# Kernel tuning notes

Hardware: AMD Instinct MI355X
Metric: run time of the kernel (lower is better)

Reference implementation:

```python
import jax, jax.numpy as jnp
import numpy as np

GROUPS = 8
NUM_HEADS = 8
EPS = 1e-5


def setup_inputs() -> dict:
    key = jax.random.key(0)
    ks = jax.random.split(key, 3)
    C = 512
    x = jax.random.normal(ks[0], (2, C, 64, 64), dtype=jnp.float32)
    norm_w = jnp.ones((C,), jnp.float32)
    norm_b = jnp.zeros((C,), jnp.float32)
    qkv_w = jax.random.normal(ks[1], (3 * C, C), dtype=jnp.float32) * (C ** -0.5)
    qkv_b = jnp.zeros((3 * C,), jnp.float32)
    proj_w = jax.random.normal(ks[2], (C, C), dtype=jnp.float32) * (C ** -0.5)
    proj_b = jnp.zeros((C,), jnp.float32)
    return {"x": x, "norm_w": norm_w, "norm_b": norm_b,
            "qkv_w": qkv_w, "qkv_b": qkv_b,
            "proj_w": proj_w, "proj_b": proj_b}


def reference(x, norm_w, norm_b, qkv_w, qkv_b, proj_w, proj_b):
    b, c, h, w = x.shape
    n = h * w
    hd = c // NUM_HEADS

    # GroupNorm(8, c): normalize over (channels-in-group, h, w)
    xg = x.reshape(b, GROUPS, c // GROUPS, h, w)
    mean = jnp.mean(xg, axis=(2, 3, 4), keepdims=True)
    var = jnp.var(xg, axis=(2, 3, 4), keepdims=True)
    xg = (xg - mean) * jax.lax.rsqrt(var + EPS)
    x_norm = xg.reshape(b, c, h, w) * norm_w[None, :, None, None] + norm_b[None, :, None, None]

    x_flat = x_norm.reshape(b, c, n)  # (b, c, n)
    # 1x1 Conv1d == channel-wise linear
    qkv = jnp.einsum('oc,bcn->bon', qkv_w, x_flat) + qkv_b[None, :, None]
    q, k, v = jnp.split(qkv, 3, axis=1)
    q = q.reshape(b, NUM_HEADS, hd, n)
    k = k.reshape(b, NUM_HEADS, hd, n)
    v = v.reshape(b, NUM_HEADS, hd, n)

    attn = jnp.einsum('bhdn,bhdm->bhnm', q, k) * (hd ** -0.5)  # (b,h,n,n)
    attn = jax.nn.softmax(attn, axis=-1)
    out = jnp.einsum('bhnm,bhdm->bhdn', attn, v).reshape(b, c, n)

    out = jnp.einsum('oc,bcn->bon', proj_w, out) + proj_b[None, :, None]
    return x + out.reshape(b, c, h, w)
```

## Files before the change

### kernel.cpp

```cpp
#include <hip/hip_runtime.h>
#include <stdint.h>

#define B_   2
#define C_   512
#define N_   4096
#define G_   8
#define NH_  8
#define HD_  64
#define GRPELEMS ((C_ / G_) * N_)
#define NCHUNK 64

typedef __bf16 bf16x8 __attribute__((ext_vector_type(8)));
typedef float  f32x4  __attribute__((ext_vector_type(4)));

#if __has_builtin(__builtin_amdgcn_exp2f)
#define EXP2(x) __builtin_amdgcn_exp2f(x)
#else
#define EXP2(x) exp2f(x)
#endif

__device__ inline unsigned f2bf(float f) {
    union { float f; unsigned u; } v; v.f = f;
    return (v.u + 0x7FFFu + ((v.u >> 16) & 1u)) >> 16;
}
__device__ inline __bf16 tobf(float f) {
    unsigned short u = (unsigned short)f2bf(f);
    union { unsigned short u; __bf16 b; } c; c.u = u;
    return c.b;
}
__device__ inline unsigned pktrunc(float f0, float f1) {
    return __builtin_amdgcn_perm(__float_as_uint(f1), __float_as_uint(f0),
                                 0x07060302u);
}

#define GLOAD16(g, l)                                                     \
    __builtin_amdgcn_global_load_lds(                                     \
        (const __attribute__((address_space(1))) unsigned*)(g),           \
        (__attribute__((address_space(3))) unsigned*)(l), 16, 0, 0)

__global__ __launch_bounds__(256) void gn_part(const float* __restrict__ x,
                                               float* __restrict__ psum,
                                               float* __restrict__ psq) {
    const int blk = blockIdx.x;
    const float4* p = (const float4*)x + (size_t)blk * 1024;
    const int t = threadIdx.x;
    float s = 0.f, s2 = 0.f;
#pragma unroll
    for (int i = 0; i < 4; ++i) {
        float4 v = p[t + (i << 8)];
        s  += v.x + v.y + v.z + v.w;
        s2 += v.x * v.x + v.y * v.y + v.z * v.z + v.w * v.w;
    }
#pragma unroll
    for (int off = 1; off < 64; off <<= 1) {
        s  += __shfl_xor(s, off);
        s2 += __shfl_xor(s2, off);
    }
    __shared__ float rs[4], rq[4];
    if ((t & 63) == 0) { rs[t >> 6] = s; rq[t >> 6] = s2; }
    __syncthreads();
    if (t == 0) {
        psum[blk] = rs[0] + rs[1] + rs[2] + rs[3];
        psq[blk]  = rq[0] + rq[1] + rq[2] + rq[3];
    }
}

__global__ __launch_bounds__(256) void w2bf(const float* __restrict__ qw,
                                            const float* __restrict__ pw,
                                            __bf16* __restrict__ dq,
                                            __bf16* __restrict__ dp) {
    const int QW4 = (3 * C_ * C_) / 4;
    int idx = blockIdx.x * 256 + threadIdx.x;
    float4 v; __bf16* dst; int o;
    if (idx < QW4) { v = ((const float4*)qw)[idx]; dst = dq; o = idx; }
    else           { v = ((const float4*)pw)[idx - QW4]; dst = dp; o = idx - QW4; }
    uint2 pk;
    pk.x = f2bf(v.x) | (f2bf(v.y) << 16);
    pk.y = f2bf(v.z) | (f2bf(v.w) << 16);
    *(uint2*)(dst + (size_t)o * 4) = pk;
}

__global__ __launch_bounds__(256) void gn_apply_t(const float* __restrict__ x,
                                                  const float* __restrict__ w,
                                                  const float* __restrict__ bb,
                                                  const float* __restrict__ psum,
                                                  const float* __restrict__ psq,
                                                  __bf16* __restrict__ xnT) {
    const int p0 = blockIdx.x << 6, c0 = blockIdx.y << 6, b = blockIdx.z;
    __shared__ __bf16 T[64][76];
    __shared__ float red[2 * NCHUNK];
    __shared__ float smr[2];
    const int tid = threadIdx.x;
    const int bg = b * G_ + (c0 >> 6);

    if (tid < NCHUNK)            red[tid] = psum[bg * NCHUNK + tid];
    else if (tid < 2 * NCHUNK)   red[tid] = psq[bg * NCHUNK + tid - NCHUNK];
    __syncthreads();
    if (tid == 0) {
        float s = 0.f, q = 0.f;
#pragma unroll
        for (int i = 0; i < NCHUNK; ++i) { s += red[i]; q += red[NCHUNK + i]; }
        const float inv = 1.f / (float)GRPELEMS;
        float mean = s * inv;
        float var  = q * inv - mean * mean;
        smr[0] = mean;
        smr[1] = rsqrtf(var + 1e-5f);
    }
    __syncthreads();
    const float mean = smr[0], rstd = smr[1];

    const int tr  = tid >> 4;
    const int tc4 = (tid & 15) << 2;
    const float* xb = x + ((size_t)b * C_ + c0) * N_ + p0;
#pragma unroll
    for (int cc = tr; cc < 64; cc += 16) {
        int c = c0 + cc;
        float sc = rstd * w[c];
        float sh = bb[c] - mean * sc;
        float4 v = *(const float4*)(xb + (size_t)cc * N_ + tc4);
        T[tc4 + 0][cc] = tobf(v.x * sc + sh);
        T[tc4 + 1][cc] = tobf(v.y * sc + sh);
        T[tc4 + 2][cc] = tobf(v.z * sc + sh);
        T[tc4 + 3][cc] = tobf(v.w * sc + sh);
    }
    __syncthreads();
    __bf16* dst = xnT + ((size_t)b * N_ + p0) * C_ + c0;
#pragma unroll
    for (int pp = tr; pp < 64; pp += 16)
        *(uint2*)(dst + (size_t)pp * C_ + tc4) = *(const uint2*)&T[pp][tc4];
}

template <int M_TOTAL, int EPI>
__global__ __launch_bounds__(256) void gemm_bf16(const __bf16* __restrict__ A,
                                                 const __bf16* __restrict__ Bm,
                                                 const float* __restrict__ bias,
                                                 const float* __restrict__ resid,
                                                 __bf16* __restrict__ qT,
                                                 __bf16* __restrict__ kT,
                                                 __bf16* __restrict__ vB,
                                                 float* __restrict__ Y) {
    const int b  = blockIdx.z;
    const int M0 = blockIdx.y << 7;
    const int N0 = blockIdx.x << 7;
    const int tid = threadIdx.x;
    const int w = tid >> 6, lane = tid & 63;
    const int quad = lane >> 4, l16 = lane & 15;
    const int wr = w >> 1, wc = w & 1;

    __shared__ __bf16 As[128 * 64];
    __shared__ __bf16 Bs[128 * 64];

    const __bf16* Bb = Bm + (size_t)b * ((size_t)N_ * C_);

    const int srow = lane >> 3;
    const int sg   = lane & 7;

    f32x4 acc[4][4];
#pragma unroll
    for (int mt = 0; mt < 4; ++mt)
#pragma unroll
        for (int nt = 0; nt < 4; ++nt) acc[mt][nt] = (f32x4){0.f, 0.f, 0.f, 0.f};

    for (int k0 = 0; k0 < C_; k0 += 64) {
        __syncthreads();
#pragma unroll
        for (int i = 0; i < 4; ++i) {
            int r  = (w << 5) + (i << 3) + srow;
            int gc = ((sg ^ (r & 7)) << 3);
            const __bf16* ga = A  + (size_t)(M0 + r) * C_ + k0 + gc;
            const __bf16* gb = Bb + (size_t)(N0 + r) * C_ + k0 + gc;
            GLOAD16(ga, As + (((w << 2) + i) << 9));
            GLOAD16(gb, Bs + (((w << 2) + i) << 9));
        }
        __syncthreads();

#pragma unroll
        for (int kk = 0; kk < 2; ++kk) {
            bf16x8 af[4], bfr[4];
            const int gk = (kk << 2) + quad;
#pragma unroll
            for (int mt = 0; mt < 4; ++mt) {
                int m = (wr << 6) + (mt << 4) + l16;
                af[mt] = *(const bf16x8*)&As[(m << 6) + ((gk ^ (m & 7)) << 3)];
            }
#pragma unroll
            for (int nt = 0; nt < 4; ++nt) {
                int n = (wc << 6) + (nt << 4) + l16;
                bfr[nt] = *(const bf16x8*)&Bs[(n << 6) + ((gk ^ (n & 7)) << 3)];
            }
#pragma unroll
            for (int mt = 0; mt < 4; ++mt)
#pragma unroll
                for (int nt = 0; nt < 4; ++nt)
                    acc[mt][nt] = __builtin_amdgcn_mfma_f32_16x16x32_bf16(
                        af[mt], bfr[nt], acc[mt][nt], 0, 0, 0);
        }
    }

    if (EPI == 0) {
        const int t = M0 >> 9;
        const float sc = (t == 0) ? (0.125f * 1.44269504f) : 1.f;
#pragma unroll
        for (int mt = 0; mt < 4; ++mt) {
            const int o0 = M0 + (wr << 6) + (mt << 4) + (quad << 2);
            const int h  = (o0 >> 6) & 7;
            const int d0 = o0 & 63;
            const size_t bh = (size_t)b * NH_ + h;
            float bi[4];
#pragma unroll
            for (int r = 0; r < 4; ++r) bi[r] = bias[o0 + r];
            if (t < 2) {
                __bf16* dst = (t == 0 ? qT : kT) + (bh * N_) * HD_ + d0;
#pragma unroll
                for (int nt = 0; nt < 4; ++nt) {
                    int p = N0 + (wc << 6) + (nt << 4) + l16;
                    f32x4 v = acc[mt][nt];
                    uint2 pk;
                    pk.x = f2bf((v[0] + bi[0]) * sc) | (f2bf((v[1] + bi[1]) * sc) << 16);
                    pk.y = f2bf((v[2] + bi[2]) * sc) | (f2bf((v[3] + bi[3]) * sc) << 16);
                    *(uint2*)(dst + (size_t)p * HD_) = pk;
                }
            } else {
                __bf16* dst = vB + bh * ((size_t)HD_ * N_);
#pragma unroll
                for (int nt = 0; nt < 4; ++nt) {
                    int p = N0 + (wc << 6) + (nt << 4) + l16;
                    f32x4 v = acc[mt][nt];
#pragma unroll
                    for (int r = 0; r < 4; ++r)
                        dst[(size_t)(d0 + r) * N_ + p] = tobf(v[r] + bi[r]);
                }
            }
        }
    } else {
#pragma unroll
        for (int mt = 0; mt < 4; ++mt) {
            const int o0 = M0 + (wr << 6) + (mt << 4) + (quad << 2);
            float bi[4];
#pragma unroll
            for (int r = 0; r < 4; ++r) bi[r] = bias[o0 + r];
#pragma unroll
            for (int nt = 0; nt < 4; ++nt) {
                int p = N0 + (wc << 6) + (nt << 4) + l16;
                f32x4 v = acc[mt][nt];
#pragma unroll
                for (int r = 0; r < 4; ++r) {
                    size_t off = ((size_t)b * C_ + o0 + r) * N_ + p;
                    Y[off] = v[r] + bi[r] + resid[off];
                }
            }
        }
    }
}

__global__ __launch_bounds__(256) void attn_mfma(const __bf16* __restrict__ qT,
                                                 const __bf16* __restrict__ kT,
                                                 const __bf16* __restrict__ vB,
                                                 __bf16* __restrict__ attT) {
    const int tid  = threadIdx.x;
    const int w    = tid >> 6;
    const int lane = tid & 63;
    const int quad = lane >> 4;
    const int l16  = lane & 15;
    const int l7   = l16 & 7;
    const int h = blockIdx.y, b = blockIdx.z;
    const int qw0 = (blockIdx.x << 7) + (w << 5);

    __shared__ __bf16 Ks[2][64][64];
    __shared__ __bf16 Vs[2][80][64];
    __shared__ __bf16 Ps[4][32][64];

    const size_t bh = (size_t)b * NH_ + h;
    const __bf16* qTb = qT + bh * ((size_t)N_ * HD_);
    const __bf16* kTb = kT + bh * ((size_t)N_ * HD_);
    const __bf16* vBb = vB + bh * ((size_t)HD_ * N_);

    {
        int r = tid >> 3;
        int c = (tid & 7) << 3;
        __bf16 val = ((r & 15) == 0) ? (__bf16)1.0f : (__bf16)0.0f;
        __bf16* dst = &Vs[r >> 4][64 + (r & 15)][c];
#pragma unroll
        for (int u = 0; u < 8; ++u) dst[u] = val;
    }

    bf16x8 qf[2][2];
#pragma unroll
    for (int qt = 0; qt < 2; ++qt)
#pragma unroll
        for (int hh = 0; hh < 2; ++hh)
            qf[qt][hh] = *(const bf16x8*)(qTb +
                (size_t)(qw0 + (qt << 4) + l16) * HD_ + (hh << 5) + (quad << 3));

    const int rrel = lane >> 3;
    const int gsw  = ((lane & 7) ^ rrel) << 3;

    auto stage = [&](int it, int buf) {
        const int kb = it << 6;
#pragma unroll
        for (int c = 0; c < 2; ++c) {
            const int rb = (w << 4) + (c << 3);
            const __bf16* gk = kTb + (size_t)(kb + rb + rrel) * HD_ + gsw;
            GLOAD16(gk, &Ks[buf][rb][0]);
            const __bf16* gv = vBb + (size_t)(rb + rrel) * N_ + kb + gsw;
            GLOAD16(gv, &Vs[buf][rb][0]);
        }
    };

    const f32x4 zero4 = {0.f, 0.f, 0.f, 0.f};
    f32x4 o[5][2];
#pragma unroll
    for (int dt = 0; dt < 5; ++dt) { o[dt][0] = zero4; o[dt][1] = zero4; }

    stage(0, 0);

    for (int it = 0; it < 64; ++it) {
        const int cur = it & 1;
        __syncthreads();
        if (it < 63) stage(it + 1, cur ^ 1);

        f32x4 s[4][2];
#pragma unroll
        for (int kt = 0; kt < 4; ++kt) { s[kt][0] = zero4; s[kt][1] = zero4; }
#pragma unroll
        for (int hh = 0; hh < 2; ++hh) {
#pragma unroll
            for (int kt = 0; kt < 4; ++kt) {
                bf16x8 a = *(const bf16x8*)&Ks[cur][(kt << 4) + l16]
                                              [(((hh << 2) + quad) ^ l7) << 3];
                s[kt][0] = __builtin_amdgcn_mfma_f32_16x16x32_bf16(a, qf[0][hh], s[kt][0], 0, 0, 0);
                s[kt][1] = __builtin_amdgcn_mfma_f32_16x16x32_bf16(a, qf[1][hh], s[kt][1], 0, 0, 0);
            }
        }

#pragma unroll
        for (int qt = 0; qt < 2; ++qt)
#pragma unroll
            for (int kt = 0; kt < 4; ++kt) {
                f32x4 sv = s[kt][qt];
                float e0 = EXP2(sv[0]), e1 = EXP2(sv[1]);
                float e2 = EXP2(sv[2]), e3 = EXP2(sv[3]);
                uint2 pk;
                pk.x = pktrunc(e0, e1);
                pk.y = pktrunc(e2, e3);
                *(uint2*)&Ps[w][(qt << 4) + l16]
                            [(((kt << 2) + quad) ^ (l7 << 1)) << 2] = pk;
            }

#pragma unroll
        for (int hh = 0; hh < 2; ++hh) {
            bf16x8 pf0 = *(const bf16x8*)&Ps[w][l16]
                          [(((hh << 3) + (quad << 1)) ^ (l7 << 1)) << 2];
            bf16x8 pf1 = *(const bf16x8*)&Ps[w][16 + l16]
                          [(((hh << 3) + (quad << 1)) ^ (l7 << 1)) << 2];
#pragma unroll
            for (int dt = 0; dt < 5; ++dt) {
                bf16x8 a = *(const bf16x8*)&Vs[cur][(dt << 4) + l16]
                                              [(((hh << 2) + quad) ^ l7) << 3];
                o[dt][0] = __builtin_amdgcn_mfma_f32_16x16x32_bf16(a, pf0, o[dt][0], 0, 0, 0);
                o[dt][1] = __builtin_amdgcn_mfma_f32_16x16x32_bf16(a, pf1, o[dt][1], 0, 0, 0);
            }
        }
    }

    float lq[2];
    lq[0] = __shfl(o[4][0][0], l16, 64);
    lq[1] = __shfl(o[4][1][0], l16, 64);

#pragma unroll
    for (int qt = 0; qt < 2; ++qt) {
        float inv = 1.f / lq[qt];
        int n = qw0 + (qt << 4) + l16;
        __bf16* dst = attT + ((size_t)b * N_ + n) * C_ + h * HD_ + (quad << 2);
#pragma unroll
        for (int dt = 0; dt < 4; ++dt) {
            uint2 pk;
            pk.x = f2bf(o[dt][qt][0] * inv) | (f2bf(o[dt][qt][1] * inv) << 16);
            pk.y = f2bf(o[dt][qt][2] * inv) | (f2bf(o[dt][qt][3] * inv) << 16);
            *(uint2*)(dst + (dt << 4)) = pk;
        }
    }
}

extern "C" void kernel_launch(void* const* d_in, const int* in_sizes, int n_in,
                              void* d_out, int out_size, void* d_ws, size_t ws_size,
                              hipStream_t stream) {
    const float* x      = (const float*)d_in[0];
    const float* norm_w = (const float*)d_in[1];
    const float* norm_b = (const float*)d_in[2];
    const float* qkv_w  = (const float*)d_in[3];
    const float* qkv_b  = (const float*)d_in[4];
    const float* proj_w = (const float*)d_in[5];
    const float* proj_b = (const float*)d_in[6];
    float* out = (float*)d_out;

    const size_t BCN = (size_t)B_ * C_ * N_;
    float* psum  = (float*)d_ws;
    float* psq   = psum + 1024;
    __bf16* xnT  = (__bf16*)(psq + 1024);
    __bf16* qT   = xnT + BCN;
    __bf16* kT   = qT + BCN;
    __bf16* vB   = kT + BCN;
    __bf16* attT = vB + BCN;
    __bf16* wq   = attT + BCN;
    __bf16* wp   = wq + (size_t)3 * C_ * C_;

    gn_part<<<B_ * G_ * NCHUNK, 256, 0, stream>>>(x, psum, psq);
    w2bf<<<(4 * C_ * C_ / 4) / 256, 256, 0, stream>>>(qkv_w, proj_w, wq, wp);
    gn_apply_t<<<dim3(N_ / 64, C_ / 64, B_), 256, 0, stream>>>(
        x, norm_w, norm_b, psum, psq, xnT);
    gemm_bf16<3 * C_, 0><<<dim3(N_ / 128, 3 * C_ / 128, B_), 256, 0, stream>>>(
        wq, xnT, qkv_b, nullptr, qT, kT, vB, nullptr);
    attn_mfma<<<dim3(N_ / 128, NH_, B_), 256, 0, stream>>>(qT, kT, vB, attT);
    gemm_bf16<C_, 1><<<dim3(N_ / 128, C_ / 128, B_), 256, 0, stream>>>(
        wp, attT, proj_b, x, nullptr, nullptr, nullptr, out);
}
```

Before: 230.6 us.

## Give each attention wave 64 queries with 2 waves per block

The attention kernel now runs 128 threads (2 waves) per block, and each wave handles 64 query rows instead of 32. Every K and V fragment read from LDS therefore feeds four MFMAs instead of two, cutting LDS reads per unit of work. Staging and the ones-row initialisation are redistributed over fewer threads. The cost is many more accumulator registers per wave (score and output tiles double), which may reduce occupancy, and half as many waves per block to hide latency.

```diff
diff --git a/kernel.cpp b/kernel.cpp
--- a/kernel.cpp
+++ b/kernel.cpp
@@ -253,7 +253,7 @@
     }
 }
 
-__global__ __launch_bounds__(256) void attn_mfma(const __bf16* __restrict__ qT,
+__global__ __launch_bounds__(128) void attn_mfma(const __bf16* __restrict__ qT,
                                                  const __bf16* __restrict__ kT,
                                                  const __bf16* __restrict__ vB,
                                                  __bf16* __restrict__ attT) {
@@ -264,29 +264,32 @@
     const int l16  = lane & 15;
     const int l7   = l16 & 7;
     const int h = blockIdx.y, b = blockIdx.z;
-    const int qw0 = (blockIdx.x << 7) + (w << 5);
+    const int qw0 = (blockIdx.x << 7) + (w << 6);
 
     __shared__ __bf16 Ks[2][64][64];
     __shared__ __bf16 Vs[2][80][64];
-    __shared__ __bf16 Ps[4][32][64];
+    __shared__ __bf16 Ps[2][64][64];
 
     const size_t bh = (size_t)b * NH_ + h;
     const __bf16* qTb = qT + bh * ((size_t)N_ * HD_);
     const __bf16* kTb = kT + bh * ((size_t)N_ * HD_);
     const __bf16* vBb = vB + bh * ((size_t)HD_ * N_);
 
-    {
-        int r = tid >> 3;
-        int c = (tid & 7) << 3;
-        __bf16 val = ((r & 15) == 0) ? (__bf16)1.0f : (__bf16)0.0f;
-        __bf16* dst = &Vs[r >> 4][64 + (r & 15)][c];
-#pragma unroll
-        for (int u = 0; u < 8; ++u) dst[u] = val;
-    }
-
-    bf16x8 qf[2][2];
-#pragma unroll
-    for (int qt = 0; qt < 2; ++qt)
+#pragma unroll
+    for (int u = 0; u < 2; ++u) {
+        int unit = (u << 7) + tid;
+        int buf = unit >> 7;
+        int row = (unit >> 3) & 15;
+        int g   = unit & 7;
+        __bf16 val = (row == 0) ? (__bf16)1.0f : (__bf16)0.0f;
+        __bf16* dst = &Vs[buf][64 + row][g << 3];
+#pragma unroll
+        for (int e = 0; e < 8; ++e) dst[e] = val;
+    }
+
+    bf16x8 qf[4][2];
+#pragma unroll
+    for (int qt = 0; qt < 4; ++qt)
 #pragma unroll
         for (int hh = 0; hh < 2; ++hh)
             qf[qt][hh] = *(const bf16x8*)(qTb +
@@ -298,8 +301,8 @@
     auto stage = [&](int it, int buf) {
         const int kb = it << 6;
 #pragma unroll
-        for (int c = 0; c < 2; ++c) {
-            const int rb = (w << 4) + (c << 3);
+        for (int c = 0; c < 4; ++c) {
+            const int rb = (w << 5) + (c << 3);
             const __bf16* gk = kTb + (size_t)(kb + rb + rrel) * HD_ + gsw;
             GLOAD16(gk, &Ks[buf][rb][0]);
             const __bf16* gv = vBb + (size_t)(rb + rrel) * N_ + kb + gsw;
@@ -308,9 +311,11 @@
     };
 
     const f32x4 zero4 = {0.f, 0.f, 0.f, 0.f};
-    f32x4 o[5][2];
-#pragma unroll
-    for (int dt = 0; dt < 5; ++dt) { o[dt][0] = zero4; o[dt][1] = zero4; }
+    f32x4 o[5][4];
+#pragma unroll
+    for (int dt = 0; dt < 5; ++dt)
+#pragma unroll
+        for (int qt = 0; qt < 4; ++qt) o[dt][qt] = zero4;
 
     stage(0, 0);
 
@@ -319,22 +324,26 @@
         __syncthreads();
         if (it < 63) stage(it + 1, cur ^ 1);
 
-        f32x4 s[4][2];
-#pragma unroll
-        for (int kt = 0; kt < 4; ++kt) { s[kt][0] = zero4; s[kt][1] = zero4; }
+        f32x4 s[4][4];
+#pragma unroll
+        for (int kt = 0; kt < 4; ++kt)
+#pragma unroll
+            for (int qt = 0; qt < 4; ++qt) s[kt][qt] = zero4;
 #pragma unroll
         for (int hh = 0; hh < 2; ++hh) {
 #pragma unroll
             for (int kt = 0; kt < 4; ++kt) {
                 bf16x8 a = *(const bf16x8*)&Ks[cur][(kt << 4) + l16]
                                               [(((hh << 2) + quad) ^ l7) << 3];
-                s[kt][0] = __builtin_amdgcn_mfma_f32_16x16x32_bf16(a, qf[0][hh], s[kt][0], 0, 0, 0);
-                s[kt][1] = __builtin_amdgcn_mfma_f32_16x16x32_bf16(a, qf[1][hh], s[kt][1], 0, 0, 0);
-            }
-        }
-
-#pragma unroll
-        for (int qt = 0; qt < 2; ++qt)
+#pragma unroll
+                for (int qt = 0; qt < 4; ++qt)
+                    s[kt][qt] = __builtin_amdgcn_mfma_f32_16x16x32_bf16(
+                        a, qf[qt][hh], s[kt][qt], 0, 0, 0);
+            }
+        }
+
+#pragma unroll
+        for (int qt = 0; qt < 4; ++qt)
 #pragma unroll
             for (int kt = 0; kt < 4; ++kt) {
                 f32x4 sv = s[kt][qt];
@@ -349,26 +358,29 @@
 
 #pragma unroll
         for (int hh = 0; hh < 2; ++hh) {
-            bf16x8 pf0 = *(const bf16x8*)&Ps[w][l16]
-                          [(((hh << 3) + (quad << 1)) ^ (l7 << 1)) << 2];
-            bf16x8 pf1 = *(const bf16x8*)&Ps[w][16 + l16]
-                          [(((hh << 3) + (quad << 1)) ^ (l7 << 1)) << 2];
+            bf16x8 pf[4];
+#pragma unroll
+            for (int qt = 0; qt < 4; ++qt)
+                pf[qt] = *(const bf16x8*)&Ps[w][(qt << 4) + l16]
+                              [(((hh << 3) + (quad << 1)) ^ (l7 << 1)) << 2];
 #pragma unroll
             for (int dt = 0; dt < 5; ++dt) {
                 bf16x8 a = *(const bf16x8*)&Vs[cur][(dt << 4) + l16]
                                               [(((hh << 2) + quad) ^ l7) << 3];
-                o[dt][0] = __builtin_amdgcn_mfma_f32_16x16x32_bf16(a, pf0, o[dt][0], 0, 0, 0);
-                o[dt][1] = __builtin_amdgcn_mfma_f32_16x16x32_bf16(a, pf1, o[dt][1], 0, 0, 0);
-            }
-        }
-    }
-
-    float lq[2];
-    lq[0] = __shfl(o[4][0][0], l16, 64);
-    lq[1] = __shfl(o[4][1][0], l16, 64);
-
-#pragma unroll
-    for (int qt = 0; qt < 2; ++qt) {
+#pragma unroll
+                for (int qt = 0; qt < 4; ++qt)
+                    o[dt][qt] = __builtin_amdgcn_mfma_f32_16x16x32_bf16(
+                        a, pf[qt], o[dt][qt], 0, 0, 0);
+            }
+        }
+    }
+
+    float lq[4];
+#pragma unroll
+    for (int qt = 0; qt < 4; ++qt) lq[qt] = __shfl(o[4][qt][0], l16, 64);
+
+#pragma unroll
+    for (int qt = 0; qt < 4; ++qt) {
         float inv = 1.f / lq[qt];
         int n = qw0 + (qt << 4) + l16;
         __bf16* dst = attT + ((size_t)b * N_ + n) * C_ + h * HD_ + (quad << 2);
@@ -411,7 +423,7 @@
         x, norm_w, norm_b, psum, psq, xnT);
     gemm_bf16<3 * C_, 0><<<dim3(N_ / 128, 3 * C_ / 128, B_), 256, 0, stream>>>(
         wq, xnT, qkv_b, nullptr, qT, kT, vB, nullptr);
-    attn_mfma<<<dim3(N_ / 128, NH_, B_), 256, 0, stream>>>(qT, kT, vB, attT);
+    attn_mfma<<<dim3(N_ / 128, NH_, B_), 128, 0, stream>>>(qT, kT, vB, attT);
     gemm_bf16<C_, 1><<<dim3(N_ / 128, C_ / 128, B_), 256, 0, stream>>>(
         wp, attT, proj_b, x, nullptr, nullptr, nullptr, out);
 }
```

Measured after the change: 259.9 us. 12.7% more time.
